# Performance work log

Hardware: AMD Instinct MI355X
Metric: run time of the kernel (lower is better)

## Reference

```python
import jax, jax.numpy as jnp
import numpy as np

B, S, E = 2, 2048, 2048
H, HD = 32, 64          # n_heads, head_dim
KV, REP = 8, 4          # n_kv_head, n_kv_head_rep (H == KV*REP)
NEG = -1e9


def setup_inputs() -> dict:
    key = jax.random.key(0)
    ks = jax.random.split(key, 6)
    x = jax.random.normal(ks[0], (B, S, E), dtype=jnp.float32)
    # Llama RoPE tables: angles[p, i] = p / 10000^(2i/HD)
    inv_freq = 1.0 / (10000.0 ** (jnp.arange(0, HD, 2, dtype=jnp.float32) / HD))
    angles = jnp.arange(S, dtype=jnp.float32)[:, None] * inv_freq[None, :]  # [S, HD/2]
    cos, sin = jnp.cos(angles), jnp.sin(angles)
    # causal additive mask [S, S]
    mask = jnp.where(jnp.tril(jnp.ones((S, S), dtype=bool)), 0.0, NEG).astype(jnp.float32)
    sc = 0.02
    wq = jax.random.normal(ks[1], (E, H * HD), dtype=jnp.float32) * sc
    wk = jax.random.normal(ks[2], (E, KV * HD), dtype=jnp.float32) * sc
    wv = jax.random.normal(ks[3], (E, KV * HD), dtype=jnp.float32) * sc
    wo = jax.random.normal(ks[4], (H * HD, E), dtype=jnp.float32) * sc
    return {"x": x, "cos": cos, "sin": sin, "mask": mask,
            "wq": wq, "wk": wk, "wv": wv, "wo": wo, "start_pos": 0}


def _rope(t, cos, sin):
    # t: [B, S, h, HD]; rotate consecutive pairs (Llama complex convention)
    tp = t.reshape(t.shape[:-1] + (HD // 2, 2))
    t1, t2 = tp[..., 0], tp[..., 1]
    c = cos[None, :, None, :]
    s = sin[None, :, None, :]
    out = jnp.stack([t1 * c - t2 * s, t1 * s + t2 * c], axis=-1)
    return out.reshape(t.shape)


def reference(x, cos, sin, mask, wq, wk, wv, wo, start_pos):
    b, s, _ = x.shape
    q = (x @ wq).reshape(b, s, H, HD)
    k = (x @ wk).reshape(b, s, KV, HD)
    v = (x @ wv).reshape(b, s, KV, HD)
    q = _rope(q, cos, sin)
    k = _rope(k, cos, sin)
    # KV-cache: with start_pos=0 and full-seq prefill, the cache slice
    # [:, :start_pos+s] is exactly the freshly written k/v, so use them directly.
    # Grouped attention without materializing repeated K/V:
    # q -> [b, KV, REP, s, HD]; k,v -> [b, KV, s, HD]
    qg = q.transpose(0, 2, 1, 3).reshape(b, KV, REP, s, HD)
    kg = k.transpose(0, 2, 1, 3)
    vg = v.transpose(0, 2, 1, 3)
    scale = 1.0 / jnp.sqrt(jnp.float32(HD))
    scores = jnp.einsum('bgrqd,bgkd->bgrqk', qg, kg) * scale + mask
    attn = jax.nn.softmax(scores, axis=-1)
    og = jnp.einsum('bgrqk,bgkd->bgrqd', attn, vg)     # [b, KV, REP, s, HD]
    out = og.reshape(b, H, s, HD).transpose(0, 2, 1, 3).reshape(b, s, H * HD)
    return out @ wo
```

## Files before the change

### kernel.cpp

```cpp
#include <hip/hip_runtime.h>
#include <stdint.h>

#define S_LEN 2048
#define NTOK  4096
#define EMB   2048
#define NHEAD 32
#define HDIM  64
#define NKVH  8

typedef __bf16 bf16x8 __attribute__((ext_vector_type(8)));
typedef float  f32x4  __attribute__((ext_vector_type(4)));

#define AS1 __attribute__((address_space(1)))
#define AS3 __attribute__((address_space(3)))

#if __has_builtin(__builtin_amdgcn_exp2f)
#define EXP2(x) __builtin_amdgcn_exp2f(x)
#else
#define EXP2(x) exp2f(x)
#endif

#define QSCALE 0.1803368867f

__device__ __forceinline__ uint16_t f2bf(float f) {
  uint32_t u = __float_as_uint(f);
  u += 0x7fffu + ((u >> 16) & 1u);
  return (uint16_t)(u >> 16);
}
__device__ __forceinline__ float bf2f(uint16_t h) {
  return __uint_as_float(((uint32_t)h) << 16);
}
__device__ __forceinline__ void gld16(const void* g, void* l) {
  __builtin_amdgcn_global_load_lds((const AS1 uint32_t*)g, (AS3 uint32_t*)l, 16, 0, 0);
}
__device__ __forceinline__ f32x4 mfma16(bf16x8 a, bf16x8 b, f32x4 c) {
  return __builtin_amdgcn_mfma_f32_16x16x32_bf16(a, b, c, 0, 0, 0);
}

__global__ void k_preproc(const float* __restrict__ x, uint16_t* __restrict__ xb,
                          const float* __restrict__ wq, const float* __restrict__ wk,
                          const float* __restrict__ wv, const float* __restrict__ wo,
                          uint16_t* __restrict__ wT, uint16_t* __restrict__ woT) {
  __shared__ float tile[32][33];
  int bid = blockIdx.x;
  if (bid < 8192) {
    int i = (bid * 256 + threadIdx.x) * 4;
    float4 v = *(const float4*)(x + i);
    ushort4 o;
    o.x = f2bf(v.x); o.y = f2bf(v.y); o.z = f2bf(v.z); o.w = f2bf(v.w);
    *(ushort4*)(xb + i) = o;
    return;
  }
  bid -= 8192;
  const float* src; uint16_t* dst; int C, bx, by;
  if (bid < 4096)      { src = wq; dst = wT;                       C = 2048; bx = bid & 63; by = bid >> 6; }
  else if (bid < 5120) { src = wk; dst = wT + (size_t)2048 * 2048; C = 512;  bid -= 4096; bx = bid & 15; by = bid >> 4; }
  else if (bid < 6144) { src = wv; dst = wT + (size_t)2560 * 2048; C = 512;  bid -= 5120; bx = bid & 15; by = bid >> 4; }
  else                 { src = wo; dst = woT;                      C = 2048; bid -= 6144; bx = bid & 63; by = bid >> 6; }
  const int R = 2048;
  int c0 = bx * 32, r0 = by * 32;
  int tx = threadIdx.x & 31, ty = threadIdx.x >> 5;
#pragma unroll
  for (int j = 0; j < 32; j += 8)
    tile[ty + j][tx] = src[(size_t)(r0 + ty + j) * C + c0 + tx];
  __syncthreads();
#pragma unroll
  for (int j = 0; j < 32; j += 8)
    dst[(size_t)(c0 + ty + j) * R + r0 + tx] = f2bf(tile[tx][ty + j]);
}

__global__ void k_transpose_v(const uint16_t* __restrict__ qkv, uint16_t* __restrict__ out) {
  __shared__ uint16_t tile[32][33];
  int s0 = blockIdx.x * 32, hd0 = blockIdx.y * 32, bh = blockIdx.z;
  int b = bh >> 3, kvh = bh & 7;
  int tx = threadIdx.x & 31, ty = threadIdx.x >> 5;
#pragma unroll
  for (int j = 0; j < 32; j += 8)
    tile[ty + j][tx] =
        qkv[((size_t)b * S_LEN + s0 + ty + j) * 3072 + 2560 + kvh * 64 + hd0 + tx];
  __syncthreads();
#pragma unroll
  for (int j = 0; j < 32; j += 8)
    out[((size_t)bh * 64 + hd0 + ty + j) * S_LEN + s0 + tx] = tile[tx][ty + j];
}

template <int N_REP, typename OUT_T>
__global__ __launch_bounds__(256, 2) void k_gemm128(
    const uint16_t* __restrict__ A, const uint16_t* __restrict__ BT,
    OUT_T* __restrict__ C, int M, int N, int K) {
  constexpr int NF = 2 * N_REP;
  constexpr int LDSH = 8192 + N_REP * 4096;
  __shared__ uint16_t lds[2][LDSH];
  const int tid = threadIdx.x, lane = tid & 63, w = tid >> 6;
  const int wm = w >> 1, wn = w & 1;
  const int l16 = lane & 15, lg = lane >> 4;
  const int nbn = N / (N_REP * 64);
  const int nwg = gridDim.x, cpx = nwg >> 3;
  const int swz = ((int)blockIdx.x & 7) * cpx + ((int)blockIdx.x >> 3);
  const int bm = (swz / nbn) * 128, bn = (swz % nbn) * (N_REP * 64);

  f32x4 acc[4][NF] = {};

  const int srow = tid >> 3, sslot = tid & 7;
  const int schunk = (sslot ^ (srow & 7)) * 8;
  const uint16_t* Ag = A + (size_t)(bm + srow) * K + schunk;
  const uint16_t* Bg = BT + (size_t)(bn + srow) * K + schunk;

  auto stageA = [&](int d, int r, int k0) {
    gld16(Ag + (size_t)r * 32 * K + k0, &lds[d][r * 2048 + tid * 8]);
  };
  auto stageB = [&](int d, int r, int k0) {
    gld16(Bg + (size_t)r * 32 * K + k0, &lds[d][8192 + r * 2048 + tid * 8]);
  };
  auto lda = [&](int d, int mf, int s) -> bf16x8 {
    int row = wm * 64 + mf * 16 + l16;
    int slot = (s * 4 + lg) ^ (row & 7);
    return *(const bf16x8*)(&lds[d][row * 64 + slot * 8]);
  };
  auto ldb = [&](int d, int nf, int s) -> bf16x8 {
    int row = wn * (N_REP * 32) + nf * 16 + l16;
    int slot = (s * 4 + lg) ^ (row & 7);
    return *(const bf16x8*)(&lds[d][8192 + row * 64 + slot * 8]);
  };

  const int NT = K >> 6;
#pragma unroll
  for (int r = 0; r < 4; ++r) stageA(0, r, 0);
#pragma unroll
  for (int r = 0; r < 2 * N_REP; ++r) stageB(0, r, 0);
#pragma unroll
  for (int r = 0; r < 4; ++r) if (1 < NT) stageA(1, r, 64);
  asm volatile("s_waitcnt vmcnt(4)" ::: "memory");
  __builtin_amdgcn_s_barrier();

  for (int kt = 0; kt < NT; ++kt) {
    const int cur = kt & 1;
    const int nk0 = (kt + 1) << 6, nnk0 = (kt + 2) << 6;
    const bool m1 = (kt + 1 < NT), m2 = (kt + 2 < NT);
    bf16x8 a[2][2], a2[2][2], b[NF][2];
#pragma unroll
    for (int mi = 0; mi < 2; ++mi) { a[mi][0] = lda(cur, mi, 0); a[mi][1] = lda(cur, mi, 1); }
#pragma unroll
    for (int ni = 0; ni < NF; ++ni) { b[ni][0] = ldb(cur, ni, 0); b[ni][1] = ldb(cur, ni, 1); }
    if (m1) {
#pragma unroll
      for (int r = 0; r < 2 * N_REP; ++r) stageB(cur ^ 1, r, nk0);
    }
    __builtin_amdgcn_s_barrier();
    asm volatile("s_waitcnt lgkmcnt(0)" ::: "memory");
    __builtin_amdgcn_sched_barrier(0);
    __builtin_amdgcn_s_setprio(1);
#pragma unroll
    for (int mi = 0; mi < 2; ++mi)
#pragma unroll
      for (int ni = 0; ni < NF; ++ni) {
        acc[mi][ni] = mfma16(a[mi][0], b[ni][0], acc[mi][ni]);
        acc[mi][ni] = mfma16(a[mi][1], b[ni][1], acc[mi][ni]);
      }
    __builtin_amdgcn_s_setprio(0);
    __builtin_amdgcn_s_barrier();
#pragma unroll
    for (int mi = 0; mi < 2; ++mi) { a2[mi][0] = lda(cur, 2 + mi, 0); a2[mi][1] = lda(cur, 2 + mi, 1); }
    __builtin_amdgcn_s_barrier();
    asm volatile("s_waitcnt lgkmcnt(0)" ::: "memory");
    __builtin_amdgcn_sched_barrier(0);
    __builtin_amdgcn_s_setprio(1);
#pragma unroll
    for (int mi = 0; mi < 2; ++mi)
#pragma unroll
      for (int ni = 0; ni < N_REP; ++ni) {
        acc[2 + mi][ni] = mfma16(a2[mi][0], b[ni][0], acc[2 + mi][ni]);
        acc[2 + mi][ni] = mfma16(a2[mi][1], b[ni][1], acc[2 + mi][ni]);
      }
    __builtin_amdgcn_s_setprio(0);
    __builtin_amdgcn_s_barrier();
    if (m2) {
#pragma unroll
      for (int r = 0; r < 4; ++r) stageA(cur, r, nnk0);
    }
    __builtin_amdgcn_s_setprio(1);
#pragma unroll
    for (int mi = 0; mi < 2; ++mi)
#pragma unroll
      for (int ni = N_REP; ni < NF; ++ni) {
        acc[2 + mi][ni] = mfma16(a2[mi][0], b[ni][0], acc[2 + mi][ni]);
        acc[2 + mi][ni] = mfma16(a2[mi][1], b[ni][1], acc[2 + mi][ni]);
      }
    __builtin_amdgcn_s_setprio(0);
    if (m2) { asm volatile("s_waitcnt vmcnt(4)" ::: "memory"); }
    else    { asm volatile("s_waitcnt vmcnt(0)" ::: "memory"); }
    __builtin_amdgcn_s_barrier();
  }
#pragma unroll
  for (int mf = 0; mf < 4; ++mf)
#pragma unroll
    for (int nf = 0; nf < NF; ++nf)
#pragma unroll
      for (int r = 0; r < 4; ++r) {
        int row = bm + wm * 64 + mf * 16 + lg * 4 + r;
        int col = bn + wn * (N_REP * 32) + nf * 16 + l16;
        float v = acc[mf][nf][r];
        if constexpr (sizeof(OUT_T) == 4) C[(size_t)row * N + col] = v;
        else                              C[(size_t)row * N + col] = f2bf(v);
      }
}

__global__ void k_rope(const uint16_t* __restrict__ qkv, const float* __restrict__ cosT,
                       const float* __restrict__ sinT, uint16_t* __restrict__ qb,
                       uint16_t* __restrict__ kb) {
  int idx = blockIdx.x * 256 + threadIdx.x;
  int row = idx / 320;
  int col8 = (idx - row * 320) * 8;
  int s = row & (S_LEN - 1);
  union { uint4 q; uint16_t u[8]; } in;
  in.q = *(const uint4*)(qkv + (size_t)row * 3072 + col8);
  const bool isQ = (col8 < 2048);
  int cc = isQ ? col8 : col8 - 2048;
  int i0 = (cc & 63) >> 1;
  float4 c4 = *(const float4*)(cosT + s * 32 + i0);
  float4 s4 = *(const float4*)(sinT + s * 32 + i0);
  if (isQ) {
    c4.x *= QSCALE; c4.y *= QSCALE; c4.z *= QSCALE; c4.w *= QSCALE;
    s4.x *= QSCALE; s4.y *= QSCALE; s4.z *= QSCALE; s4.w *= QSCALE;
  }
  float cs[4] = {c4.x, c4.y, c4.z, c4.w};
  float sn[4] = {s4.x, s4.y, s4.z, s4.w};
  union { uint4 q; uint16_t u[8]; } out;
#pragma unroll
  for (int p = 0; p < 4; ++p) {
    float t1 = bf2f(in.u[2 * p]), t2 = bf2f(in.u[2 * p + 1]);
    out.u[2 * p]     = f2bf(t1 * cs[p] - t2 * sn[p]);
    out.u[2 * p + 1] = f2bf(t1 * sn[p] + t2 * cs[p]);
  }
  if (isQ) *(uint4*)(qb + (size_t)row * 2048 + col8) = out.q;
  else     *(uint4*)(kb + (size_t)row * 512 + cc)    = out.q;
}

template <bool MASKED>
__device__ __forceinline__ void tile_compute(
    const uint16_t* Kc, const uint16_t* Vc, const bf16x8 qf[2][2], bf16x8 onesv,
    int l16, int lg, int kv0, int qb0,
    float m_r[2], f32x4 lacc[2], f32x4 acc[2][4]) {
  f32x4 st[2][4] = {};
  __builtin_amdgcn_s_setprio(1);
#pragma unroll
  for (int c = 0; c < 4; ++c) {
    int row = c * 16 + l16, sw = row & 7;
    bf16x8 ka  = *(const bf16x8*)(Kc + row * 64 + ((lg ^ sw) * 8));
    bf16x8 kb2 = *(const bf16x8*)(Kc + row * 64 + (((4 | lg) ^ sw) * 8));
#pragma unroll
    for (int qc = 0; qc < 2; ++qc) {
      st[qc][c] = mfma16(ka,  qf[qc][0], st[qc][c]);
      st[qc][c] = mfma16(kb2, qf[qc][1], st[qc][c]);
    }
  }
  __builtin_amdgcn_s_setprio(0);
  bf16x8 pu[2][2];
#pragma unroll
  for (int qc = 0; qc < 2; ++qc) {
    const int qrow = qb0 + qc * 16 + l16;
    float sv[4][4];
#pragma unroll
    for (int c = 0; c < 4; ++c)
#pragma unroll
      for (int r = 0; r < 4; ++r) {
        float s = st[qc][c][r];
        if (MASKED && (kv0 + c * 16 + lg * 4 + r > qrow)) s = -1e30f;
        sv[c][r] = s;
      }
    float mx = fmaxf(sv[0][0], sv[0][1]);
    mx = fmaxf(fmaxf(mx, sv[0][2]), sv[0][3]);
    mx = fmaxf(fmaxf(mx, sv[1][0]), sv[1][1]);
    mx = fmaxf(fmaxf(mx, sv[1][2]), sv[1][3]);
    mx = fmaxf(fmaxf(mx, sv[2][0]), sv[2][1]);
    mx = fmaxf(fmaxf(mx, sv[2][2]), sv[2][3]);
    mx = fmaxf(fmaxf(mx, sv[3][0]), sv[3][1]);
    mx = fmaxf(fmaxf(mx, sv[3][2]), sv[3][3]);
    if (!__all(mx - m_r[qc] <= 8.0f)) {
      float mxf = fmaxf(mx, __shfl_xor(mx, 16));
      mxf = fmaxf(mxf, __shfl_xor(mxf, 32));
      float m_new = fmaxf(m_r[qc], mxf);
      float alpha = EXP2(m_r[qc] - m_new);
      float al[4];
#pragma unroll
      for (int r = 0; r < 4; ++r) al[r] = __shfl(alpha, lg * 4 + r);
#pragma unroll
      for (int n = 0; n < 4; ++n)
#pragma unroll
        for (int r = 0; r < 4; ++r) acc[qc][n][r] *= al[r];
#pragma unroll
      for (int r = 0; r < 4; ++r) lacc[qc][r] *= al[r];
      m_r[qc] = m_new;
    }
    float pf[4][4];
#pragma unroll
    for (int c = 0; c < 4; ++c)
#pragma unroll
      for (int r = 0; r < 4; ++r)
        pf[c][r] = EXP2(sv[c][r] - m_r[qc]);
#pragma unroll
    for (int cc = 0; cc < 2; ++cc)
#pragma unroll
      for (int e = 0; e < 8; ++e)
        ((__bf16*)&pu[qc][cc])[e] = (__bf16)pf[cc * 2 + (e >> 2)][e & 3];
  }
  __builtin_amdgcn_s_setprio(1);
#pragma unroll
  for (int cc = 0; cc < 2; ++cc) {
    lacc[0] = mfma16(pu[0][cc], onesv, lacc[0]);
    lacc[1] = mfma16(pu[1][cc], onesv, lacc[1]);
#pragma unroll
    for (int n = 0; n < 4; ++n) {
      int row = n * 16 + l16, sw2 = row & 7;
      int k0 = cc * 32 + lg * 4, k1 = k0 + 16;
      const char* base = (const char*)Vc + row * 128;
      union { uint64_t q[2]; bf16x8 v; } vu;
      vu.q[0] = *(const uint64_t*)(base + (((k0 >> 3) ^ sw2) << 4) + ((k0 & 7) << 1));
      vu.q[1] = *(const uint64_t*)(base + (((k1 >> 3) ^ sw2) << 4) + ((k1 & 7) << 1));
      acc[0][n] = mfma16(pu[0][cc], vu.v, acc[0][n]);
      acc[1][n] = mfma16(pu[1][cc], vu.v, acc[1][n]);
    }
  }
  __builtin_amdgcn_s_setprio(0);
}

__global__ __launch_bounds__(256, 3) void k_flash(
    const uint16_t* __restrict__ Qb, const uint16_t* __restrict__ Kb,
    const uint16_t* __restrict__ VT, uint16_t* __restrict__ Ob) {
  __shared__ uint16_t Ks[3][4096];
  __shared__ uint16_t Vs[3][4096];
  const int j = 63 - ((int)blockIdx.x >> 4);
  const int gb = blockIdx.x & 15;
  const int g = gb & 7, b = gb >> 3;
  const int tid = threadIdx.x, lane = tid & 63, w = tid >> 6;
  const int l16 = lane & 15, lg = lane >> 4;
  const int h = g * 4 + w;
  const int qb0 = j * 32;

  bf16x8 qf[2][2];
#pragma unroll
  for (int qc = 0; qc < 2; ++qc) {
    const size_t tokq = (size_t)b * S_LEN + qb0 + qc * 16 + l16;
    qf[qc][0] = *(const bf16x8*)(Qb + tokq * 2048 + h * 64 + lg * 8);
    qf[qc][1] = *(const bf16x8*)(Qb + tokq * 2048 + h * 64 + 32 + lg * 8);
  }
  bf16x8 onesv;
#pragma unroll
  for (int e = 0; e < 8; ++e) ((__bf16*)&onesv)[e] = (__bf16)1.0f;

  const int srow = tid >> 3, shc = tid & 7;
  const int swz = (shc ^ (srow & 7)) * 8;
  const uint16_t* Kg = Kb + ((size_t)b * S_LEN + srow) * 512 + g * 64 + swz;
  const uint16_t* Vg = VT + ((size_t)(b * 8 + g) * 64 + srow) * S_LEN + swz;

  float m_r[2] = {-1e30f, -1e30f};
  f32x4 lacc[2] = {};
  f32x4 acc[2][4] = {};
  const int nt = (j >> 1) + 1;

  auto stage = [&](int t, int buf) {
    const size_t kv0 = (size_t)t * 64;
    uint16_t* kd = &Ks[buf][tid * 8];
    uint16_t* vd = &Vs[buf][tid * 8];
    gld16(Kg + kv0 * 512, kd);
    gld16(Kg + (kv0 + 32) * 512, kd + 2048);
    gld16(Vg + kv0, vd);
    gld16(Vg + kv0 + (size_t)32 * S_LEN, vd + 2048);
  };

  stage(0, 0);
  stage(nt > 1 ? 1 : 0, 1);

  int cur = 0;
  for (int t = 0; t < nt; ++t) {
    asm volatile("s_waitcnt vmcnt(4)" ::: "memory");
    __builtin_amdgcn_s_barrier();
    {
      int ts = t + 2 < nt ? t + 2 : nt - 1;
      int bufn = cur + 2; if (bufn >= 3) bufn -= 3;
      stage(ts, bufn);
    }
    if (t == nt - 1)
      tile_compute<true >(Ks[cur], Vs[cur], qf, onesv, l16, lg, t * 64, qb0, m_r, lacc, acc);
    else
      tile_compute<false>(Ks[cur], Vs[cur], qf, onesv, l16, lg, t * 64, qb0, m_r, lacc, acc);
    cur = cur + 1 < 3 ? cur + 1 : 0;
  }
#pragma unroll
  for (int qc = 0; qc < 2; ++qc) {
    float li[4];
#pragma unroll
    for (int r = 0; r < 4; ++r) li[r] = 1.0f / lacc[qc][r];
#pragma unroll
    for (int n = 0; n < 4; ++n)
#pragma unroll
      for (int r = 0; r < 4; ++r) {
        int qo = qb0 + qc * 16 + lg * 4 + r;
        Ob[((size_t)b * S_LEN + qo) * 2048 + h * 64 + n * 16 + l16] =
            f2bf(acc[qc][n][r] * li[r]);
      }
  }
}

extern "C" void kernel_launch(void* const* d_in, const int* in_sizes, int n_in,
                              void* d_out, int out_size, void* d_ws, size_t ws_size,
                              hipStream_t stream) {
  const float* x    = (const float*)d_in[0];
  const float* cosT = (const float*)d_in[1];
  const float* sinT = (const float*)d_in[2];
  const float* wq   = (const float*)d_in[4];
  const float* wk   = (const float*)d_in[5];
  const float* wv   = (const float*)d_in[6];
  const float* wo   = (const float*)d_in[7];
  float* out = (float*)d_out;

  char* ws = (char*)d_ws;
  size_t off = 0;
  auto alloc = [&](size_t bytes) {
    void* p = ws + off;
    off += (bytes + 255) & ~(size_t)255;
    return p;
  };
  uint16_t* xb   = (uint16_t*)alloc((size_t)NTOK * EMB * 2);
  uint16_t* wT   = (uint16_t*)alloc((size_t)3072 * 2048 * 2);
  uint16_t* woT  = (uint16_t*)alloc((size_t)2048 * 2048 * 2);
  uint16_t* qkvb = (uint16_t*)alloc((size_t)NTOK * 3072 * 2);
  uint16_t* qb   = (uint16_t*)alloc((size_t)NTOK * 2048 * 2);
  uint16_t* kb   = (uint16_t*)alloc((size_t)NTOK * 512 * 2);
  uint16_t* vT   = (uint16_t*)alloc((size_t)NTOK * 512 * 2);
  uint16_t* ob   = xb;

  k_preproc<<<18432, 256, 0, stream>>>(x, xb, wq, wk, wv, wo, wT, woT);

  k_gemm128<3, uint16_t><<<512, 256, 0, stream>>>(xb, wT, qkvb, 4096, 3072, 2048);
  k_rope<<<(NTOK * 320) / 256, 256, 0, stream>>>(qkvb, cosT, sinT, qb, kb);
  k_transpose_v<<<dim3(64, 2, 16), 256, 0, stream>>>(qkvb, vT);
  k_flash<<<dim3(1024), 256, 0, stream>>>(qb, kb, vT, ob);
  k_gemm128<2, float><<<512, 256, 0, stream>>>(ob, woT, out, 4096, 2048, 2048);
}
```

Measured before the change: 164.4 us.

## Double flash query tile to 64 rows and merge RoPE with V transpose

The flash attention kernel now processes 64 query rows per block instead of 32. This halves the grid to 512 blocks and reuses each staged K/V tile across twice as many MFMAs, with a new causal ordering that pairs long and short blocks. Separately, the RoPE and V-transpose kernels are merged into one launch to drop a kernel boundary. The cost is more accumulator registers (launch bounds drop from 3 to 2 blocks per CU), fewer blocks in flight, and possible load imbalance across the causal triangle.

```diff
diff --git a/kernel.cpp b/kernel.cpp
--- a/kernel.cpp
+++ b/kernel.cpp
@@ -67,21 +67,6 @@
 #pragma unroll
   for (int j = 0; j < 32; j += 8)
     dst[(size_t)(c0 + ty + j) * R + r0 + tx] = f2bf(tile[tx][ty + j]);
-}
-
-__global__ void k_transpose_v(const uint16_t* __restrict__ qkv, uint16_t* __restrict__ out) {
-  __shared__ uint16_t tile[32][33];
-  int s0 = blockIdx.x * 32, hd0 = blockIdx.y * 32, bh = blockIdx.z;
-  int b = bh >> 3, kvh = bh & 7;
-  int tx = threadIdx.x & 31, ty = threadIdx.x >> 5;
-#pragma unroll
-  for (int j = 0; j < 32; j += 8)
-    tile[ty + j][tx] =
-        qkv[((size_t)b * S_LEN + s0 + ty + j) * 3072 + 2560 + kvh * 64 + hd0 + tx];
-  __syncthreads();
-#pragma unroll
-  for (int j = 0; j < 32; j += 8)
-    out[((size_t)bh * 64 + hd0 + ty + j) * S_LEN + s0 + tx] = tile[tx][ty + j];
 }
 
 template <int N_REP, typename OUT_T>
@@ -205,43 +190,60 @@
       }
 }
 
-__global__ void k_rope(const uint16_t* __restrict__ qkv, const float* __restrict__ cosT,
-                       const float* __restrict__ sinT, uint16_t* __restrict__ qb,
-                       uint16_t* __restrict__ kb) {
-  int idx = blockIdx.x * 256 + threadIdx.x;
-  int row = idx / 320;
-  int col8 = (idx - row * 320) * 8;
-  int s = row & (S_LEN - 1);
-  union { uint4 q; uint16_t u[8]; } in;
-  in.q = *(const uint4*)(qkv + (size_t)row * 3072 + col8);
-  const bool isQ = (col8 < 2048);
-  int cc = isQ ? col8 : col8 - 2048;
-  int i0 = (cc & 63) >> 1;
-  float4 c4 = *(const float4*)(cosT + s * 32 + i0);
-  float4 s4 = *(const float4*)(sinT + s * 32 + i0);
-  if (isQ) {
-    c4.x *= QSCALE; c4.y *= QSCALE; c4.z *= QSCALE; c4.w *= QSCALE;
-    s4.x *= QSCALE; s4.y *= QSCALE; s4.z *= QSCALE; s4.w *= QSCALE;
-  }
-  float cs[4] = {c4.x, c4.y, c4.z, c4.w};
-  float sn[4] = {s4.x, s4.y, s4.z, s4.w};
-  union { uint4 q; uint16_t u[8]; } out;
-#pragma unroll
-  for (int p = 0; p < 4; ++p) {
-    float t1 = bf2f(in.u[2 * p]), t2 = bf2f(in.u[2 * p + 1]);
-    out.u[2 * p]     = f2bf(t1 * cs[p] - t2 * sn[p]);
-    out.u[2 * p + 1] = f2bf(t1 * sn[p] + t2 * cs[p]);
-  }
-  if (isQ) *(uint4*)(qb + (size_t)row * 2048 + col8) = out.q;
-  else     *(uint4*)(kb + (size_t)row * 512 + cc)    = out.q;
+__global__ void k_rope_tv(const uint16_t* __restrict__ qkv, const float* __restrict__ cosT,
+                          const float* __restrict__ sinT, uint16_t* __restrict__ qb,
+                          uint16_t* __restrict__ kb, uint16_t* __restrict__ vT) {
+  int bid = blockIdx.x;
+  if (bid < 5120) {
+    int idx = bid * 256 + threadIdx.x;
+    int row = idx / 320;
+    int col8 = (idx - row * 320) * 8;
+    int s = row & (S_LEN - 1);
+    union { uint4 q; uint16_t u[8]; } in;
+    in.q = *(const uint4*)(qkv + (size_t)row * 3072 + col8);
+    const bool isQ = (col8 < 2048);
+    int cc = isQ ? col8 : col8 - 2048;
+    int i0 = (cc & 63) >> 1;
+    float4 c4 = *(const float4*)(cosT + s * 32 + i0);
+    float4 s4 = *(const float4*)(sinT + s * 32 + i0);
+    if (isQ) {
+      c4.x *= QSCALE; c4.y *= QSCALE; c4.z *= QSCALE; c4.w *= QSCALE;
+      s4.x *= QSCALE; s4.y *= QSCALE; s4.z *= QSCALE; s4.w *= QSCALE;
+    }
+    float cs[4] = {c4.x, c4.y, c4.z, c4.w};
+    float sn[4] = {s4.x, s4.y, s4.z, s4.w};
+    union { uint4 q; uint16_t u[8]; } out;
+#pragma unroll
+    for (int p = 0; p < 4; ++p) {
+      float t1 = bf2f(in.u[2 * p]), t2 = bf2f(in.u[2 * p + 1]);
+      out.u[2 * p]     = f2bf(t1 * cs[p] - t2 * sn[p]);
+      out.u[2 * p + 1] = f2bf(t1 * sn[p] + t2 * cs[p]);
+    }
+    if (isQ) *(uint4*)(qb + (size_t)row * 2048 + col8) = out.q;
+    else     *(uint4*)(kb + (size_t)row * 512 + cc)    = out.q;
+    return;
+  }
+  __shared__ uint16_t tile[32][33];
+  bid -= 5120;
+  int s0 = (bid & 63) * 32, hd0 = ((bid >> 6) & 1) * 32, bh = bid >> 7;
+  int b = bh >> 3, kvh = bh & 7;
+  int tx = threadIdx.x & 31, ty = threadIdx.x >> 5;
+#pragma unroll
+  for (int j = 0; j < 32; j += 8)
+    tile[ty + j][tx] =
+        qkv[((size_t)b * S_LEN + s0 + ty + j) * 3072 + 2560 + kvh * 64 + hd0 + tx];
+  __syncthreads();
+#pragma unroll
+  for (int j = 0; j < 32; j += 8)
+    vT[((size_t)bh * 64 + hd0 + ty + j) * S_LEN + s0 + tx] = tile[tx][ty + j];
 }
 
 template <bool MASKED>
-__device__ __forceinline__ void tile_compute(
-    const uint16_t* Kc, const uint16_t* Vc, const bf16x8 qf[2][2], bf16x8 onesv,
+__device__ __forceinline__ void tile_compute4(
+    const uint16_t* Kc, const uint16_t* Vc, const bf16x8 qf[4][2], bf16x8 onesv,
     int l16, int lg, int kv0, int qb0,
-    float m_r[2], f32x4 lacc[2], f32x4 acc[2][4]) {
-  f32x4 st[2][4] = {};
+    float m_r[4], f32x4 lacc[4], f32x4 acc[4][4]) {
+  f32x4 st[4][4] = {};
   __builtin_amdgcn_s_setprio(1);
 #pragma unroll
   for (int c = 0; c < 4; ++c) {
@@ -249,15 +251,15 @@
     bf16x8 ka  = *(const bf16x8*)(Kc + row * 64 + ((lg ^ sw) * 8));
     bf16x8 kb2 = *(const bf16x8*)(Kc + row * 64 + (((4 | lg) ^ sw) * 8));
 #pragma unroll
-    for (int qc = 0; qc < 2; ++qc) {
+    for (int qc = 0; qc < 4; ++qc) {
       st[qc][c] = mfma16(ka,  qf[qc][0], st[qc][c]);
       st[qc][c] = mfma16(kb2, qf[qc][1], st[qc][c]);
     }
   }
   __builtin_amdgcn_s_setprio(0);
-  bf16x8 pu[2][2];
-#pragma unroll
-  for (int qc = 0; qc < 2; ++qc) {
+  bf16x8 pu[4][2];
+#pragma unroll
+  for (int qc = 0; qc < 4; ++qc) {
     const int qrow = qb0 + qc * 16 + l16;
     float sv[4][4];
 #pragma unroll
@@ -307,8 +309,8 @@
   __builtin_amdgcn_s_setprio(1);
 #pragma unroll
   for (int cc = 0; cc < 2; ++cc) {
-    lacc[0] = mfma16(pu[0][cc], onesv, lacc[0]);
-    lacc[1] = mfma16(pu[1][cc], onesv, lacc[1]);
+#pragma unroll
+    for (int qc = 0; qc < 4; ++qc) lacc[qc] = mfma16(pu[qc][cc], onesv, lacc[qc]);
 #pragma unroll
     for (int n = 0; n < 4; ++n) {
       int row = n * 16 + l16, sw2 = row & 7;
@@ -317,29 +319,31 @@
       union { uint64_t q[2]; bf16x8 v; } vu;
       vu.q[0] = *(const uint64_t*)(base + (((k0 >> 3) ^ sw2) << 4) + ((k0 & 7) << 1));
       vu.q[1] = *(const uint64_t*)(base + (((k1 >> 3) ^ sw2) << 4) + ((k1 & 7) << 1));
-      acc[0][n] = mfma16(pu[0][cc], vu.v, acc[0][n]);
-      acc[1][n] = mfma16(pu[1][cc], vu.v, acc[1][n]);
+#pragma unroll
+      for (int qc = 0; qc < 4; ++qc) acc[qc][n] = mfma16(pu[qc][cc], vu.v, acc[qc][n]);
     }
   }
   __builtin_amdgcn_s_setprio(0);
 }
 
-__global__ __launch_bounds__(256, 3) void k_flash(
+__global__ __launch_bounds__(256, 2) void k_flash(
     const uint16_t* __restrict__ Qb, const uint16_t* __restrict__ Kb,
     const uint16_t* __restrict__ VT, uint16_t* __restrict__ Ob) {
   __shared__ uint16_t Ks[3][4096];
   __shared__ uint16_t Vs[3][4096];
-  const int j = 63 - ((int)blockIdx.x >> 4);
-  const int gb = blockIdx.x & 15;
-  const int g = gb & 7, b = gb >> 3;
+  const int lidx = blockIdx.x;
+  const int jj = lidx & 31;
+  const int j = (lidx < 256) ? 31 - jj : jj;
+  const int gb = lidx >> 5;
+  const int g = gb & 7, b = (gb >> 3) & 1;
   const int tid = threadIdx.x, lane = tid & 63, w = tid >> 6;
   const int l16 = lane & 15, lg = lane >> 4;
   const int h = g * 4 + w;
-  const int qb0 = j * 32;
-
-  bf16x8 qf[2][2];
-#pragma unroll
-  for (int qc = 0; qc < 2; ++qc) {
+  const int qb0 = j * 64;
+
+  bf16x8 qf[4][2];
+#pragma unroll
+  for (int qc = 0; qc < 4; ++qc) {
     const size_t tokq = (size_t)b * S_LEN + qb0 + qc * 16 + l16;
     qf[qc][0] = *(const bf16x8*)(Qb + tokq * 2048 + h * 64 + lg * 8);
     qf[qc][1] = *(const bf16x8*)(Qb + tokq * 2048 + h * 64 + 32 + lg * 8);
@@ -353,10 +357,10 @@
   const uint16_t* Kg = Kb + ((size_t)b * S_LEN + srow) * 512 + g * 64 + swz;
   const uint16_t* Vg = VT + ((size_t)(b * 8 + g) * 64 + srow) * S_LEN + swz;
 
-  float m_r[2] = {-1e30f, -1e30f};
-  f32x4 lacc[2] = {};
-  f32x4 acc[2][4] = {};
-  const int nt = (j >> 1) + 1;
+  float m_r[4] = {-1e30f, -1e30f, -1e30f, -1e30f};
+  f32x4 lacc[4] = {};
+  f32x4 acc[4][4] = {};
+  const int nt = j + 1;
 
   auto stage = [&](int t, int buf) {
     const size_t kv0 = (size_t)t * 64;
@@ -381,13 +385,13 @@
       stage(ts, bufn);
     }
     if (t == nt - 1)
-      tile_compute<true >(Ks[cur], Vs[cur], qf, onesv, l16, lg, t * 64, qb0, m_r, lacc, acc);
+      tile_compute4<true >(Ks[cur], Vs[cur], qf, onesv, l16, lg, t * 64, qb0, m_r, lacc, acc);
     else
-      tile_compute<false>(Ks[cur], Vs[cur], qf, onesv, l16, lg, t * 64, qb0, m_r, lacc, acc);
+      tile_compute4<false>(Ks[cur], Vs[cur], qf, onesv, l16, lg, t * 64, qb0, m_r, lacc, acc);
     cur = cur + 1 < 3 ? cur + 1 : 0;
   }
 #pragma unroll
-  for (int qc = 0; qc < 2; ++qc) {
+  for (int qc = 0; qc < 4; ++qc) {
     float li[4];
 #pragma unroll
     for (int r = 0; r < 4; ++r) li[r] = 1.0f / lacc[qc][r];
@@ -433,8 +437,7 @@
   k_preproc<<<18432, 256, 0, stream>>>(x, xb, wq, wk, wv, wo, wT, woT);
 
   k_gemm128<3, uint16_t><<<512, 256, 0, stream>>>(xb, wT, qkvb, 4096, 3072, 2048);
-  k_rope<<<(NTOK * 320) / 256, 256, 0, stream>>>(qkvb, cosT, sinT, qb, kb);
-  k_transpose_v<<<dim3(64, 2, 16), 256, 0, stream>>>(qkvb, vT);
-  k_flash<<<dim3(1024), 256, 0, stream>>>(qb, kb, vT, ob);
+  k_rope_tv<<<5120 + 2048, 256, 0, stream>>>(qkvb, cosT, sinT, qb, kb, vT);
+  k_flash<<<dim3(512), 256, 0, stream>>>(qb, kb, vT, ob);
   k_gemm128<2, float><<<512, 256, 0, stream>>>(ob, woT, out, 4096, 2048, 2048);
 }
```

After: 355.5 us. +116.2%, slower.
